# Kernel tuning notes

Measured on AMD Instinct MI355X. Metric: run time of the kernel, lower is better.

The kernel has to match this reference:

```python
import jax, jax.numpy as jnp
import numpy as np


def setup_inputs() -> dict:
    key = jax.random.key(0)
    k1, k2, k3, k4, k5 = jax.random.split(key, 5)
    N, IN, OUT = 4096, 2048, 2048
    return {
        "input": jax.random.normal(k1, (N, IN), dtype=jnp.float32),
        "weight_mu": jax.random.normal(k2, (OUT, IN), dtype=jnp.float32) * 0.25,
        "weight_rho": jax.random.normal(k3, (OUT, IN), dtype=jnp.float32) - 5.0,
        "eps_weight": jax.random.normal(k4, (OUT, IN), dtype=jnp.float32),
        "bias": jax.random.normal(k5, (OUT,), dtype=jnp.float32) * 0.02,
    }


def reference(input, weight_mu, weight_rho, eps_weight, bias):
    # Effective weight: mu + softplus(rho) * eps   (log1p(exp(rho)) == softplus)
    w = weight_mu + jax.nn.softplus(weight_rho) * eps_weight  # [out, in]
    # F.linear: input @ w.T + bias
    return jnp.einsum("ni,oi->no", input, w) + bias
```

## Files before the change

### kernel.cpp

```cpp
#include <hip/hip_runtime.h>
#include <stdint.h>

typedef __bf16 bf16x8 __attribute__((ext_vector_type(8)));
typedef float f32x4 __attribute__((ext_vector_type(4)));
typedef float float4v __attribute__((ext_vector_type(4)));
typedef unsigned short u16x8 __attribute__((ext_vector_type(8)));

__device__ __forceinline__ unsigned short f2bf(float f) {
    unsigned u = __float_as_uint(f);
    u += 0x7fffu + ((u >> 16) & 1u);
    return (unsigned short)(u >> 16);
}

__device__ __forceinline__ float softplus(float x) {
    float ax = fabsf(x);
    return fmaxf(x, 0.0f) + log1pf(__expf(-ax));
}

__device__ __forceinline__ void gl_lds16(const void* gptr, void* lptr) {
    auto g = reinterpret_cast<const __attribute__((address_space(1))) void*>(
        reinterpret_cast<uintptr_t>(gptr));
    auto l = reinterpret_cast<__attribute__((address_space(3))) void*>(
        reinterpret_cast<uintptr_t>(lptr));
    __builtin_amdgcn_global_load_lds(g, l, 16, 0, 0);
}

__global__ void cvt_input_kernel(const float* __restrict__ in,
                                 unsigned short* __restrict__ out, int n8) {
    int i = blockIdx.x * blockDim.x + threadIdx.x;
    if (i >= n8) return;
    const float4v* p = (const float4v*)in + (size_t)i * 2;
    float4v a = p[0], b = p[1];
    u16x8 r;
    r[0] = f2bf(a[0]); r[1] = f2bf(a[1]); r[2] = f2bf(a[2]); r[3] = f2bf(a[3]);
    r[4] = f2bf(b[0]); r[5] = f2bf(b[1]); r[6] = f2bf(b[2]); r[7] = f2bf(b[3]);
    ((u16x8*)out)[i] = r;
}

__global__ void prep_w_kernel(const float* __restrict__ mu,
                              const float* __restrict__ rho,
                              const float* __restrict__ eps,
                              unsigned short* __restrict__ out, int n8) {
    int i = blockIdx.x * blockDim.x + threadIdx.x;
    if (i >= n8) return;
    const float4v* pm = (const float4v*)mu  + (size_t)i * 2;
    const float4v* pr = (const float4v*)rho + (size_t)i * 2;
    const float4v* pe = (const float4v*)eps + (size_t)i * 2;
    float4v m0 = pm[0], m1 = pm[1];
    float4v r0 = pr[0], r1 = pr[1];
    float4v e0 = pe[0], e1 = pe[1];
    u16x8 r;
    r[0] = f2bf(m0[0] + softplus(r0[0]) * e0[0]);
    r[1] = f2bf(m0[1] + softplus(r0[1]) * e0[1]);
    r[2] = f2bf(m0[2] + softplus(r0[2]) * e0[2]);
    r[3] = f2bf(m0[3] + softplus(r0[3]) * e0[3]);
    r[4] = f2bf(m1[0] + softplus(r1[0]) * e1[0]);
    r[5] = f2bf(m1[1] + softplus(r1[1]) * e1[1]);
    r[6] = f2bf(m1[2] + softplus(r1[2]) * e1[2]);
    r[7] = f2bf(m1[3] + softplus(r1[3]) * e1[3]);
    ((u16x8*)out)[i] = r;
}

#define BM 128
#define BN 128
#define BK 32

__global__ __launch_bounds__(256)
void gemm_bt_kernel(const unsigned short* __restrict__ A,
                    const unsigned short* __restrict__ B,
                    const float* __restrict__ bias,
                    float* __restrict__ C,
                    int M, int N, int K) {
    __shared__ unsigned short lds_a[BM * BK];
    __shared__ unsigned short lds_b[BN * BK];

    const int t      = threadIdx.x;
    const int lane   = t & 63;
    const int wave   = t >> 6;
    const int lane16 = lane & 15;
    const int quad   = lane >> 4;
    const int wm     = wave & 1;
    const int wn     = wave >> 1;

    const int m0 = blockIdx.y * BM;
    const int n0 = blockIdx.x * BN;

    const int srow = t >> 2;
    const int skg  = (t & 3) * 8;

    const unsigned short* Ab = A + (size_t)m0 * K;
    const unsigned short* Bb = B + (size_t)n0 * K;

    f32x4 acc[4][4] = {};

    for (int k0 = 0; k0 < K; k0 += BK) {
        gl_lds16(Ab + (size_t)srow * K        + k0 + skg, lds_a + t * 8);
        gl_lds16(Ab + (size_t)(srow + 64) * K + k0 + skg, lds_a + 2048 + t * 8);
        gl_lds16(Bb + (size_t)srow * K        + k0 + skg, lds_b + t * 8);
        gl_lds16(Bb + (size_t)(srow + 64) * K + k0 + skg, lds_b + 2048 + t * 8);
        __syncthreads();

        bf16x8 af[4], bfr[4];
#pragma unroll
        for (int mi = 0; mi < 4; mi++)
            af[mi] = *(const bf16x8*)(lds_a + (wm * 64 + mi * 16 + lane16) * BK + quad * 8);
#pragma unroll
        for (int ni = 0; ni < 4; ni++)
            bfr[ni] = *(const bf16x8*)(lds_b + (wn * 64 + ni * 16 + lane16) * BK + quad * 8);

#pragma unroll
        for (int mi = 0; mi < 4; mi++)
#pragma unroll
            for (int ni = 0; ni < 4; ni++)
                acc[mi][ni] = __builtin_amdgcn_mfma_f32_16x16x32_bf16(
                    af[mi], bfr[ni], acc[mi][ni], 0, 0, 0);
        __syncthreads();
    }

    float bv[4];
#pragma unroll
    for (int ni = 0; ni < 4; ni++)
        bv[ni] = bias[n0 + wn * 64 + ni * 16 + lane16];

#pragma unroll
    for (int mi = 0; mi < 4; mi++) {
        const int rbase = m0 + wm * 64 + mi * 16 + quad * 4;
#pragma unroll
        for (int ni = 0; ni < 4; ni++) {
            const int col = n0 + wn * 64 + ni * 16 + lane16;
#pragma unroll
            for (int r = 0; r < 4; r++)
                C[(size_t)(rbase + r) * N + col] = acc[mi][ni][r] + bv[ni];
        }
    }
}

extern "C" void kernel_launch(void* const* d_in, const int* in_sizes, int n_in,
                              void* d_out, int out_size, void* d_ws, size_t ws_size,
                              hipStream_t stream) {
    const float* input = (const float*)d_in[0];
    const float* mu    = (const float*)d_in[1];
    const float* rho   = (const float*)d_in[2];
    const float* eps   = (const float*)d_in[3];
    const float* bias  = (const float*)d_in[4];
    float* out = (float*)d_out;

    const int OUT = in_sizes[4];
    const int IN  = in_sizes[1] / OUT;
    const int M   = in_sizes[0] / IN;

    unsigned short* in_bf = (unsigned short*)d_ws;
    unsigned short* w_bf  = in_bf + (size_t)M * IN;

    {
        int n8 = (M * IN) / 8;
        cvt_input_kernel<<<dim3((n8 + 255) / 256), 256, 0, stream>>>(input, in_bf, n8);
    }
    {
        int n8 = (OUT * IN) / 8;
        prep_w_kernel<<<dim3((n8 + 255) / 256), 256, 0, stream>>>(mu, rho, eps, w_bf, n8);
    }
    gemm_bt_kernel<<<dim3(OUT / BN, M / BM), 256, 0, stream>>>(
        in_bf, w_bf, bias, out, M, OUT, IN);
}
```

Measured before the change: 180.8 us.

## Merge prep kernels, use BK=64 with XOR-swizzled LDS and 512-thread GEMM blocks

Merges the input cast and the weight prep into one launch, which saves a kernel launch and the gap between the two. The GEMM now uses BK=64 with an XOR swizzle on the LDS layout to avoid bank conflicts. Blocks grow to 8 waves, each computing a 64x32 tile, so there are more waves for latency hiding and fewer LDS round-trips per K step. Softplus now uses a faster __logf form, which is slightly less accurate for large |x|.

Measured after the change: 161.4 us. 10.7% less time.

```diff
diff --git a/kernel.cpp b/kernel.cpp
--- a/kernel.cpp
+++ b/kernel.cpp
@@ -13,8 +13,7 @@
 }
 
 __device__ __forceinline__ float softplus(float x) {
-    float ax = fabsf(x);
-    return fmaxf(x, 0.0f) + log1pf(__expf(-ax));
+    return fmaxf(x, 0.0f) + __logf(1.0f + __expf(-fabsf(x)));
 }
 
 __device__ __forceinline__ void gl_lds16(const void* gptr, void* lptr) {
@@ -25,47 +24,48 @@
     __builtin_amdgcn_global_load_lds(g, l, 16, 0, 0);
 }
 
-__global__ void cvt_input_kernel(const float* __restrict__ in,
-                                 unsigned short* __restrict__ out, int n8) {
+__global__ void prep_kernel(const float* __restrict__ in,
+                            const float* __restrict__ mu,
+                            const float* __restrict__ rho,
+                            const float* __restrict__ eps,
+                            unsigned short* __restrict__ in_bf,
+                            unsigned short* __restrict__ w_bf,
+                            int nIn8, int nW8) {
     int i = blockIdx.x * blockDim.x + threadIdx.x;
-    if (i >= n8) return;
-    const float4v* p = (const float4v*)in + (size_t)i * 2;
-    float4v a = p[0], b = p[1];
-    u16x8 r;
-    r[0] = f2bf(a[0]); r[1] = f2bf(a[1]); r[2] = f2bf(a[2]); r[3] = f2bf(a[3]);
-    r[4] = f2bf(b[0]); r[5] = f2bf(b[1]); r[6] = f2bf(b[2]); r[7] = f2bf(b[3]);
-    ((u16x8*)out)[i] = r;
-}
-
-__global__ void prep_w_kernel(const float* __restrict__ mu,
-                              const float* __restrict__ rho,
-                              const float* __restrict__ eps,
-                              unsigned short* __restrict__ out, int n8) {
-    int i = blockIdx.x * blockDim.x + threadIdx.x;
-    if (i >= n8) return;
-    const float4v* pm = (const float4v*)mu  + (size_t)i * 2;
-    const float4v* pr = (const float4v*)rho + (size_t)i * 2;
-    const float4v* pe = (const float4v*)eps + (size_t)i * 2;
-    float4v m0 = pm[0], m1 = pm[1];
-    float4v r0 = pr[0], r1 = pr[1];
-    float4v e0 = pe[0], e1 = pe[1];
-    u16x8 r;
-    r[0] = f2bf(m0[0] + softplus(r0[0]) * e0[0]);
-    r[1] = f2bf(m0[1] + softplus(r0[1]) * e0[1]);
-    r[2] = f2bf(m0[2] + softplus(r0[2]) * e0[2]);
-    r[3] = f2bf(m0[3] + softplus(r0[3]) * e0[3]);
-    r[4] = f2bf(m1[0] + softplus(r1[0]) * e1[0]);
-    r[5] = f2bf(m1[1] + softplus(r1[1]) * e1[1]);
-    r[6] = f2bf(m1[2] + softplus(r1[2]) * e1[2]);
-    r[7] = f2bf(m1[3] + softplus(r1[3]) * e1[3]);
-    ((u16x8*)out)[i] = r;
+    if (i < nIn8) {
+        const float4v* p = (const float4v*)in + (size_t)i * 2;
+        float4v a = p[0], b = p[1];
+        u16x8 r;
+        r[0] = f2bf(a[0]); r[1] = f2bf(a[1]); r[2] = f2bf(a[2]); r[3] = f2bf(a[3]);
+        r[4] = f2bf(b[0]); r[5] = f2bf(b[1]); r[6] = f2bf(b[2]); r[7] = f2bf(b[3]);
+        ((u16x8*)in_bf)[i] = r;
+    } else {
+        int j = i - nIn8;
+        if (j >= nW8) return;
+        const float4v* pm = (const float4v*)mu  + (size_t)j * 2;
+        const float4v* pr = (const float4v*)rho + (size_t)j * 2;
+        const float4v* pe = (const float4v*)eps + (size_t)j * 2;
+        float4v m0 = pm[0], m1 = pm[1];
+        float4v r0 = pr[0], r1 = pr[1];
+        float4v e0 = pe[0], e1 = pe[1];
+        u16x8 r;
+        r[0] = f2bf(m0[0] + softplus(r0[0]) * e0[0]);
+        r[1] = f2bf(m0[1] + softplus(r0[1]) * e0[1]);
+        r[2] = f2bf(m0[2] + softplus(r0[2]) * e0[2]);
+        r[3] = f2bf(m0[3] + softplus(r0[3]) * e0[3]);
+        r[4] = f2bf(m1[0] + softplus(r1[0]) * e1[0]);
+        r[5] = f2bf(m1[1] + softplus(r1[1]) * e1[1]);
+        r[6] = f2bf(m1[2] + softplus(r1[2]) * e1[2]);
+        r[7] = f2bf(m1[3] + softplus(r1[3]) * e1[3]);
+        ((u16x8*)w_bf)[j] = r;
+    }
 }
 
 #define BM 128
 #define BN 128
-#define BK 32
+#define BK 64
 
-__global__ __launch_bounds__(256)
+__global__ __launch_bounds__(512, 4)
 void gemm_bt_kernel(const unsigned short* __restrict__ A,
                     const unsigned short* __restrict__ B,
                     const float* __restrict__ bias,
@@ -85,49 +85,58 @@
     const int m0 = blockIdx.y * BM;
     const int n0 = blockIdx.x * BN;
 
-    const int srow = t >> 2;
-    const int skg  = (t & 3) * 8;
+    const int r1   = t >> 3;
+    const int pkg1 = t & 7;
+    const int g1   = (pkg1 ^ (r1 & 7)) * 8;
+    const int r2   = r1 + 64;
+    const int g2   = (pkg1 ^ (r2 & 7)) * 8;
 
     const unsigned short* Ab = A + (size_t)m0 * K;
     const unsigned short* Bb = B + (size_t)n0 * K;
 
-    f32x4 acc[4][4] = {};
+    f32x4 acc[4][2] = {};
+
+    const int sw = lane16 & 7;
 
     for (int k0 = 0; k0 < K; k0 += BK) {
-        gl_lds16(Ab + (size_t)srow * K        + k0 + skg, lds_a + t * 8);
-        gl_lds16(Ab + (size_t)(srow + 64) * K + k0 + skg, lds_a + 2048 + t * 8);
-        gl_lds16(Bb + (size_t)srow * K        + k0 + skg, lds_b + t * 8);
-        gl_lds16(Bb + (size_t)(srow + 64) * K + k0 + skg, lds_b + 2048 + t * 8);
+        gl_lds16(Ab + (size_t)r1 * K + k0 + g1, lds_a + t * 8);
+        gl_lds16(Ab + (size_t)r2 * K + k0 + g2, lds_a + 4096 + t * 8);
+        gl_lds16(Bb + (size_t)r1 * K + k0 + g1, lds_b + t * 8);
+        gl_lds16(Bb + (size_t)r2 * K + k0 + g2, lds_b + 4096 + t * 8);
         __syncthreads();
 
-        bf16x8 af[4], bfr[4];
 #pragma unroll
-        for (int mi = 0; mi < 4; mi++)
-            af[mi] = *(const bf16x8*)(lds_a + (wm * 64 + mi * 16 + lane16) * BK + quad * 8);
+        for (int ch = 0; ch < 2; ch++) {
+            const int kg = ch * 4 + quad;
+            const int pk = (kg ^ sw) * 8;
+            bf16x8 af[4], bfr[2];
 #pragma unroll
-        for (int ni = 0; ni < 4; ni++)
-            bfr[ni] = *(const bf16x8*)(lds_b + (wn * 64 + ni * 16 + lane16) * BK + quad * 8);
-
+            for (int mi = 0; mi < 4; mi++)
+                af[mi] = *(const bf16x8*)(lds_a + (wm * 64 + mi * 16 + lane16) * BK + pk);
 #pragma unroll
-        for (int mi = 0; mi < 4; mi++)
+            for (int ni = 0; ni < 2; ni++)
+                bfr[ni] = *(const bf16x8*)(lds_b + (wn * 32 + ni * 16 + lane16) * BK + pk);
 #pragma unroll
-            for (int ni = 0; ni < 4; ni++)
-                acc[mi][ni] = __builtin_amdgcn_mfma_f32_16x16x32_bf16(
-                    af[mi], bfr[ni], acc[mi][ni], 0, 0, 0);
+            for (int mi = 0; mi < 4; mi++)
+#pragma unroll
+                for (int ni = 0; ni < 2; ni++)
+                    acc[mi][ni] = __builtin_amdgcn_mfma_f32_16x16x32_bf16(
+                        af[mi], bfr[ni], acc[mi][ni], 0, 0, 0);
+        }
         __syncthreads();
     }
 
-    float bv[4];
+    float bv[2];
 #pragma unroll
-    for (int ni = 0; ni < 4; ni++)
-        bv[ni] = bias[n0 + wn * 64 + ni * 16 + lane16];
+    for (int ni = 0; ni < 2; ni++)
+        bv[ni] = bias[n0 + wn * 32 + ni * 16 + lane16];
 
 #pragma unroll
     for (int mi = 0; mi < 4; mi++) {
         const int rbase = m0 + wm * 64 + mi * 16 + quad * 4;
 #pragma unroll
-        for (int ni = 0; ni < 4; ni++) {
-            const int col = n0 + wn * 64 + ni * 16 + lane16;
+        for (int ni = 0; ni < 2; ni++) {
+            const int col = n0 + wn * 32 + ni * 16 + lane16;
 #pragma unroll
             for (int r = 0; r < 4; r++)
                 C[(size_t)(rbase + r) * N + col] = acc[mi][ni][r] + bv[ni];
@@ -152,14 +161,11 @@
     unsigned short* in_bf = (unsigned short*)d_ws;
     unsigned short* w_bf  = in_bf + (size_t)M * IN;
 
-    {
-        int n8 = (M * IN) / 8;
-        cvt_input_kernel<<<dim3((n8 + 255) / 256), 256, 0, stream>>>(input, in_bf, n8);
-    }
-    {
-        int n8 = (OUT * IN) / 8;
-        prep_w_kernel<<<dim3((n8 + 255) / 256), 256, 0, stream>>>(mu, rho, eps, w_bf, n8);
-    }
-    gemm_bt_kernel<<<dim3(OUT / BN, M / BM), 256, 0, stream>>>(
+    const int nIn8 = (M * IN) / 8;
+    const int nW8  = (OUT * IN) / 8;
+    prep_kernel<<<dim3((nIn8 + nW8 + 255) / 256), 256, 0, stream>>>(
+        input, mu, rho, eps, in_bf, w_bf, nIn8, nW8);
+
+    gemm_bt_kernel<<<dim3(OUT / BN, M / BM), 512, 0, stream>>>(
         in_bf, w_bf, bias, out, M, OUT, IN);
 }
```
